# Kernel tuning notes

Measured on AMD Instinct MI355X. Metric: run time of the kernel, lower is better.

The kernel has to match this reference:

```python
import jax, jax.numpy as jnp
import numpy as np
import math

D_MODEL = 2048
N_HEADS = 16
D_K = D_MODEL // N_HEADS


def setup_inputs() -> dict:
    key = jax.random.key(0)
    k0, k1, k2, k3, k4 = jax.random.split(key, 5)
    B, T = 2, 2048
    x = jax.random.normal(k0, (B, T, D_MODEL), dtype=jnp.float32)
    s = 1.0 / math.sqrt(D_MODEL)
    W_qkv = jax.random.normal(k1, (3 * D_MODEL, D_MODEL), dtype=jnp.float32) * s
    b_qkv = jax.random.normal(k2, (3 * D_MODEL,), dtype=jnp.float32) * 0.01
    W_out = jax.random.normal(k3, (D_MODEL, D_MODEL), dtype=jnp.float32) * s
    b_out = jax.random.normal(k4, (D_MODEL,), dtype=jnp.float32) * 0.01
    return {"x": x, "W_qkv": W_qkv, "b_qkv": b_qkv, "W_out": W_out, "b_out": b_out}


def reference(x, W_qkv, b_qkv, W_out, b_out):
    B, T, C = x.shape
    qkv = x @ W_qkv.T + b_qkv                      # [B,T,3C]
    q, k, v = jnp.split(qkv, 3, axis=-1)
    # [B,T,C] -> [B,H,T,Dk]
    def to_heads(t):
        return t.reshape(B, T, N_HEADS, D_K).transpose(0, 2, 1, 3)
    q, k, v = to_heads(q), to_heads(k), to_heads(v)
    scale = 1.0 / math.sqrt(D_K)
    scores = jnp.einsum('bhqd,bhkd->bhqk', q, k) * scale   # [B,H,T,T]
    causal = jnp.tril(jnp.ones((T, T), dtype=bool))
    neg = jnp.finfo(scores.dtype).min
    scores = jnp.where(causal[None, None], scores, neg)
    attn = jax.nn.softmax(scores, axis=-1)
    out = jnp.einsum('bhqk,bhkd->bhqd', attn, v)           # [B,H,T,Dk]
    out = out.transpose(0, 2, 1, 3).reshape(B, T, C)
    return out @ W_out.T + b_out
```

## Files before the change

### kernel.cpp

```cpp
#include <hip/hip_runtime.h>
#include <stdint.h>

typedef short bf16x8 __attribute__((ext_vector_type(8)));
typedef float f32x4 __attribute__((ext_vector_type(4)));
typedef float f32x16 __attribute__((ext_vector_type(16)));
typedef unsigned short u16;
typedef unsigned int u32;

__device__ __forceinline__ u16 f2bf(float f) {
    u32 x = __float_as_uint(f);
    x += 0x7fffu + ((x >> 16) & 1u);
    return (u16)(x >> 16);
}
__device__ __forceinline__ u32 pack_bf2(float a, float b) {
    return (u32)f2bf(a) | ((u32)f2bf(b) << 16);
}
__device__ __forceinline__ float bf2f(u16 v) {
    return __uint_as_float(((u32)v) << 16);
}

union Frag4 { u32 u[4]; bf16x8 v; };

__device__ __forceinline__ void gload16(const u16* g, u16* l) {
    __builtin_amdgcn_global_load_lds(
        (__attribute__((address_space(1))) void*)g,
        (__attribute__((address_space(3))) void*)l,
        16, 0, 0);
}

__global__ void cvt_f32_bf16(const float* __restrict__ in, u16* __restrict__ out, long n8) {
    long stride = (long)gridDim.x * blockDim.x;
    for (long i = (long)blockIdx.x * blockDim.x + threadIdx.x; i < n8; i += stride) {
        const float4* p = (const float4*)(in + i * 8);
        float4 a = p[0], b = p[1];
        uint4 o;
        o.x = pack_bf2(a.x, a.y);
        o.y = pack_bf2(a.z, a.w);
        o.z = pack_bf2(b.x, b.y);
        o.w = pack_bf2(b.z, b.w);
        ((uint4*)out)[i] = o;
    }
}

__global__ __launch_bounds__(512, 2) void gemm128_8w(
    const u16* __restrict__ A, const u16* __restrict__ B,
    const float* __restrict__ bias, u16* __restrict__ out,
    int K, int ldo, int gxsh)
{
    __shared__ __align__(16) u16 lA[2 * 128 * 64];
    __shared__ __align__(16) u16 lB[2 * 128 * 64];
    const int tid  = threadIdx.x;
    const int lane = tid & 63;
    const int w    = tid >> 6;
    const int wm = (w >> 2) * 64;
    const int wn = (w & 3) * 32;

    const int nwg = gridDim.x;
    const int bid = blockIdx.x;
    const int swz = (bid & 7) * (nwg >> 3) + (bid >> 3);
    const int bm = (swz & ((1 << gxsh) - 1)) * 128;
    const int bn = (swz >> gxsh) * 128;

    const int lr = lane >> 3;
    const u32 sb = (u32)((lane & 7) * 16);
    const int NT = K >> 6;

    auto stage = [&](int bb, int k0) {
#pragma unroll
        for (int i = 0; i < 2; ++i) {
            const int c = w * 2 + i;
            const int row = c * 8 + lr;
            const u32 col = (sb ^ ((u32)(row & 7) << 4)) >> 1;
            gload16(A + (size_t)(bm + row) * K + k0 + col, lA + bb * 8192 + c * 512);
            gload16(B + (size_t)(bn + row) * K + k0 + col, lB + bb * 8192 + c * 512);
        }
    };

    f32x4 acc[4][2];
#pragma unroll
    for (int i = 0; i < 4; ++i)
#pragma unroll
        for (int j = 0; j < 2; ++j)
#pragma unroll
            for (int r = 0; r < 4; ++r) acc[i][j][r] = 0.f;

    stage(0, 0);
    stage(1, 64);
    asm volatile("s_waitcnt vmcnt(4)" ::: "memory");
    __builtin_amdgcn_sched_barrier(0);
    __builtin_amdgcn_s_barrier();
    __builtin_amdgcn_sched_barrier(0);

    for (int t = 0; t < NT; ++t) {
        const int cur = t & 1;
        const char* pA = (const char*)(lA + cur * 8192);
        const char* pB = (const char*)(lB + cur * 8192);
#pragma unroll
        for (int kk = 0; kk < 2; ++kk) {
            bf16x8 af[4], bfr[2];
#pragma unroll
            for (int f = 0; f < 4; ++f) {
                const int m = wm + f * 16 + (lane & 15);
                const u32 byt = (u32)(kk * 64 + (lane >> 4) * 16) ^ ((u32)(m & 7) << 4);
                af[f] = *(const bf16x8*)(pA + m * 128 + byt);
            }
#pragma unroll
            for (int j = 0; j < 2; ++j) {
                const int n = wn + j * 16 + (lane & 15);
                const u32 byt = (u32)(kk * 64 + (lane >> 4) * 16) ^ ((u32)(n & 7) << 4);
                bfr[j] = *(const bf16x8*)(pB + n * 128 + byt);
            }
            __builtin_amdgcn_s_setprio(1);
#pragma unroll
            for (int i = 0; i < 4; ++i)
#pragma unroll
                for (int j = 0; j < 2; ++j)
                    acc[i][j] = __builtin_amdgcn_mfma_f32_16x16x32_bf16(af[i], bfr[j], acc[i][j], 0, 0, 0);
            __builtin_amdgcn_s_setprio(0);
        }
        __builtin_amdgcn_sched_barrier(0);
        __builtin_amdgcn_s_barrier();
        __builtin_amdgcn_sched_barrier(0);
        if (t + 2 < NT) {
            stage(cur, (t + 2) * 64);
            asm volatile("s_waitcnt vmcnt(4)" ::: "memory");
        } else {
            asm volatile("s_waitcnt vmcnt(0)" ::: "memory");
        }
        __builtin_amdgcn_sched_barrier(0);
        __builtin_amdgcn_s_barrier();
        __builtin_amdgcn_sched_barrier(0);
    }

#pragma unroll
    for (int i = 0; i < 4; ++i) {
        int m0 = bm + wm + i * 16 + ((lane >> 4) << 2);
#pragma unroll
        for (int j = 0; j < 2; ++j) {
            int n = bn + wn + j * 16 + (lane & 15);
            float bv = bias[n];
#pragma unroll
            for (int r = 0; r < 4; ++r)
                out[(size_t)(m0 + r) * ldo + n] = f2bf(acc[i][j][r] + bv);
        }
    }
}

template<int OBF>
__global__ __launch_bounds__(256, 2) void gemm_nt(
    const u16* __restrict__ A, const u16* __restrict__ B,
    const float* __restrict__ bias, void* __restrict__ out,
    int K, int ldo, int gxsh)
{
    __shared__ __align__(16) u16 lA[2 * 128 * 64];
    __shared__ __align__(16) u16 lB[2 * 128 * 64];
    const int tid  = threadIdx.x;
    const int lane = tid & 63;
    const int w    = tid >> 6;
    const int wm = (w >> 1) * 64, wn = (w & 1) * 64;

    const int nwg = gridDim.x;
    const int bid = blockIdx.x;
    const int swz = (bid & 7) * (nwg >> 3) + (bid >> 3);
    const int bm = (swz & ((1 << gxsh) - 1)) * 128;
    const int bn = (swz >> gxsh) * 128;

    const int lr = lane >> 3;
    const u32 sb = (u32)((lane & 7) * 16);
    const int NT = K >> 6;

    auto stage = [&](int bb, int k0) {
#pragma unroll
        for (int i = 0; i < 4; ++i) {
            const int c = w * 4 + i;
            const int row = c * 8 + lr;
            const u32 col = (sb ^ ((u32)(row & 7) << 4)) >> 1;
            gload16(A + (size_t)(bm + row) * K + k0 + col, lA + bb * 8192 + c * 512);
            gload16(B + (size_t)(bn + row) * K + k0 + col, lB + bb * 8192 + c * 512);
        }
    };

    f32x4 acc[4][4];
#pragma unroll
    for (int i = 0; i < 4; ++i)
#pragma unroll
        for (int j = 0; j < 4; ++j)
#pragma unroll
            for (int r = 0; r < 4; ++r) acc[i][j][r] = 0.f;

    stage(0, 0);
    stage(1, 64);
    asm volatile("s_waitcnt vmcnt(8)" ::: "memory");
    __builtin_amdgcn_sched_barrier(0);
    __builtin_amdgcn_s_barrier();
    __builtin_amdgcn_sched_barrier(0);

    for (int t = 0; t < NT; ++t) {
        const int cur = t & 1;
        const char* pA = (const char*)(lA + cur * 8192);
        const char* pB = (const char*)(lB + cur * 8192);
#pragma unroll
        for (int kk = 0; kk < 2; ++kk) {
            bf16x8 af[4], bfr[4];
#pragma unroll
            for (int f = 0; f < 4; ++f) {
                const int m = wm + f * 16 + (lane & 15);
                const u32 byt = (u32)(kk * 64 + (lane >> 4) * 16) ^ ((u32)(m & 7) << 4);
                af[f]  = *(const bf16x8*)(pA + m * 128 + byt);
                const int n = wn + f * 16 + (lane & 15);
                const u32 bytb = (u32)(kk * 64 + (lane >> 4) * 16) ^ ((u32)(n & 7) << 4);
                bfr[f] = *(const bf16x8*)(pB + n * 128 + bytb);
            }
            __builtin_amdgcn_s_setprio(1);
#pragma unroll
            for (int i = 0; i < 4; ++i)
#pragma unroll
                for (int j = 0; j < 4; ++j)
                    acc[i][j] = __builtin_amdgcn_mfma_f32_16x16x32_bf16(af[i], bfr[j], acc[i][j], 0, 0, 0);
            __builtin_amdgcn_s_setprio(0);
        }
        __builtin_amdgcn_sched_barrier(0);
        __builtin_amdgcn_s_barrier();
        __builtin_amdgcn_sched_barrier(0);
        if (t + 2 < NT) {
            stage(cur, (t + 2) * 64);
            asm volatile("s_waitcnt vmcnt(8)" ::: "memory");
        } else {
            asm volatile("s_waitcnt vmcnt(0)" ::: "memory");
        }
        __builtin_amdgcn_sched_barrier(0);
        __builtin_amdgcn_s_barrier();
        __builtin_amdgcn_sched_barrier(0);
    }

#pragma unroll
    for (int i = 0; i < 4; ++i) {
        int m0 = bm + wm + i * 16 + ((lane >> 4) << 2);
#pragma unroll
        for (int j = 0; j < 4; ++j) {
            int n = bn + wn + j * 16 + (lane & 15);
            float bv = bias[n];
#pragma unroll
            for (int r = 0; r < 4; ++r) {
                float v = acc[i][j][r] + bv;
                if constexpr (OBF != 0)
                    ((u16*)out)[(size_t)(m0 + r) * ldo + n] = f2bf(v);
                else
                    ((float*)out)[(size_t)(m0 + r) * ldo + n] = v;
            }
        }
    }
}

__global__ __launch_bounds__(256) void transpose_v(
    const u16* __restrict__ qkv, u16* __restrict__ vt)
{
    __shared__ u16 lt[64 * 64];
    const int tid = threadIdx.x;
    const int bid = blockIdx.x;
    const int tt    = bid & 31;
    const int dtile = (bid >> 5) & 1;
    const int h     = (bid >> 6) & 15;
    const int b     = bid >> 10;
    const u16* src = qkv + ((size_t)b * 2048 + tt * 64) * 6144 + 4096 + h * 128 + dtile * 64;

    const int r = tid >> 2, ce = (tid & 3) * 16;
    uint4 a0 = *(const uint4*)(src + (size_t)r * 6144 + ce);
    uint4 a1 = *(const uint4*)(src + (size_t)r * 6144 + ce + 8);
    const u32 swz = (u32)((r & 7) << 4);
    *(uint4*)((char*)lt + r * 128 + (((u32)(ce * 2)) ^ swz)) = a0;
    *(uint4*)((char*)lt + r * 128 + (((u32)(ce * 2 + 16)) ^ swz)) = a1;
    __syncthreads();

    const int d = tid >> 2;
    u16* dst = vt + ((size_t)(b * 16 + h) * 128 + dtile * 64 + d) * 2048 + tt * 64;
#pragma unroll
    for (int it = 0; it < 2; ++it) {
        const int t0 = (tid & 3) * 8 + it * 32;
        union { u16 hh[8]; uint4 q4; } u;
#pragma unroll
        for (int uu = 0; uu < 8; ++uu) {
            int trow = t0 + uu;
            u32 byt = (u32)(trow * 128) + (((u32)(d * 2)) ^ ((u32)((trow & 7) << 4)));
            u.hh[uu] = *(const u16*)((const char*)lt + byt);
        }
        *(uint4*)(dst + t0) = u.q4;
    }
}

__constant__ unsigned char QT_TAB[30] = {11,11, 5,15,15,15,10,10,14,14,14, 9, 9, 4,13,13,13,12,12,12, 8, 8, 7, 7, 3, 6, 6, 2, 1, 0};
__constant__ unsigned char TLO_TAB[30]= { 0,24, 0, 0,22,43, 0,22, 0,20,40, 0,20, 0, 0,19,38, 0,18,36, 0,18, 0,16, 0, 0,14, 0, 0, 0};
__constant__ unsigned char THI_TAB[30]= {24,48,24,22,43,64,22,44,20,40,60,20,40,20,19,38,56,18,36,52,18,36,16,32,16,14,28,12, 8, 4};
__constant__ unsigned char SL_TAB[30] = {10,11,255,21,22,23, 8, 9,18,19,20, 6, 7,255,15,16,17,12,13,14, 4, 5, 2, 3,255, 0, 1,255,255,255};

__global__ __launch_bounds__(256) void attn_fwd(
    const u16* __restrict__ qkv, const u16* __restrict__ vt,
    u16* __restrict__ obuf, u16* __restrict__ pout, float* __restrict__ pml)
{
    __shared__ __align__(16) u16 lS[17408];
    const int tid  = threadIdx.x;
    const int lane = tid & 63;
    const int w    = tid >> 6;
    const int g    = lane >> 5;
    const int ql   = lane & 31;

    const int bid  = blockIdx.x;
    const int item = bid >> 5;
    const int bh   = bid & 31;
    const int qt   = QT_TAB[item];
    const int slot = SL_TAB[item];
    const int t_lo = TLO_TAB[item];
    const int t_hi = THI_TAB[item];
    const int b = bh >> 4, h = bh & 15;
    const size_t rowbase = (size_t)b * 2048;
    const int qb = qt * 128;
    const int qw = qb + w * 32;
    const int q  = qw + ql;

    const u16* Khead = qkv + rowbase * 6144 + 2048 + h * 128;
    const u16* Vth   = vt + (size_t)bh * 128 * 2048;

    bf16x8 qf[8];
    {
        const u16* qrow = qkv + (rowbase + q) * 6144 + h * 128;
#pragma unroll
        for (int ch = 0; ch < 8; ++ch)
            qf[ch] = *(const bf16x8*)(qrow + ch * 16 + g * 8);
    }

    f32x16 acc[4];
#pragma unroll
    for (int dt = 0; dt < 4; ++dt)
#pragma unroll
        for (int r = 0; r < 16; ++r) acc[dt][r] = 0.f;

    float m_run = -1e30f, l_run = 0.f;
    const float C2 = 0.08838834764831845f * 1.44269504088896341f;

    auto stage = [&](int bb, int t) {
        const int kb = t * 32;
#pragma unroll
        for (int i = 0; i < 2; ++i) {
            const int c = w * 2 + i;
            const int kr = c * 4 + (lane >> 4);
            const u32 kcol = (((u32)((lane & 15) * 16)) ^ ((u32)(kr & 7) << 4)) >> 1;
            gload16(Khead + (size_t)(kb + kr) * 6144 + kcol,
                    lS + bb * 4096 + c * 512);
            const int vr = c * 16 + (lane >> 2);
            const u32 vcol = (((u32)((lane & 3) * 16)) ^ ((u32)(vr & 3) << 4)) >> 1;
            gload16(Vth + (size_t)vr * 2048 + kb + vcol,
                    lS + 8192 + bb * 4096 + c * 512);
        }
    };

    stage(0, t_lo);
    __syncthreads();
    int buf = 0;

    for (int t = t_lo; t < t_hi; ++t) {
        const int kb = t * 32;
        if (t + 1 < t_hi) stage(buf ^ 1, t + 1);

        if (kb <= qw + 31) {
            const char* lKb = (const char*)(lS + buf * 4096);
            const char* lVb = (const char*)(lS + 8192 + buf * 4096);
            const bool diag = (kb == qw);

            bf16x8 kf[8];
            const u32 ksw = ((u32)ql & 7) << 4;
#pragma unroll
            for (int ch = 0; ch < 8; ++ch)
                kf[ch] = *(const bf16x8*)(lKb + ql * 256 + (((u32)(ch * 32 + g * 16)) ^ ksw));

            f32x16 s_;
#pragma unroll
            for (int r = 0; r < 16; ++r) s_[r] = 0.f;
            __builtin_amdgcn_s_setprio(1);
#pragma unroll
            for (int ch = 0; ch < 8; ++ch)
                s_ = __builtin_amdgcn_mfma_f32_32x32x16_bf16(kf[ch], qf[ch], s_, 0, 0, 0);
            __builtin_amdgcn_s_setprio(0);

            float p[16];
            float tmax = -1e30f;
#pragma unroll
            for (int r = 0; r < 16; ++r) {
                int crow = (r & 3) + 8 * (r >> 2) + 4 * g;
                float v = s_[r];
                if (diag && (crow > ql)) v = -1e30f;
                p[r] = v;
                tmax = fmaxf(tmax, v);
            }
            tmax = fmaxf(tmax, __shfl_xor(tmax, 32));
            if (!__all(tmax <= m_run + 8.0f)) {
                float mnew  = fmaxf(m_run, tmax);
                float alpha = exp2f((m_run - mnew) * C2);
#pragma unroll
                for (int dt = 0; dt < 4; ++dt) acc[dt] = acc[dt] * alpha;
                l_run *= alpha;
                m_run = mnew;
            }
            float ssum = 0.f;
#pragma unroll
            for (int r = 0; r < 16; ++r) {
                float e = exp2f((p[r] - m_run) * C2);
                p[r] = e;
                ssum += e;
            }
            ssum += __shfl_xor(ssum, 32);
            l_run += ssum;

            u32 wb[8], sw[8];
#pragma unroll
            for (int j = 0; j < 8; ++j) wb[j] = pack_bf2(p[2 * j], p[2 * j + 1]);
#pragma unroll
            for (int j = 0; j < 8; ++j) sw[j] = __shfl_xor(wb[j], 32);
            Frag4 pf0, pf1;
#pragma unroll
            for (int u = 0; u < 4; ++u) {
                const bool own = (g == (u >> 1));
                pf0.u[u] = own ? wb[2 * g + (u & 1)]     : sw[2 * g + (u & 1)];
                pf1.u[u] = own ? wb[4 + 2 * g + (u & 1)] : sw[4 + 2 * g + (u & 1)];
            }

            __builtin_amdgcn_s_setprio(1);
#pragma unroll
            for (int dt = 0; dt < 4; ++dt) {
                const u32 vrow = (u32)(dt * 32 + ql);
                const u32 vsw = (vrow & 3) << 4;
                bf16x8 v0 = *(const bf16x8*)(lVb + vrow * 64 + (((u32)(g * 16)) ^ vsw));
                bf16x8 v1 = *(const bf16x8*)(lVb + vrow * 64 + (((u32)(32 + g * 16)) ^ vsw));
                acc[dt] = __builtin_amdgcn_mfma_f32_32x32x16_bf16(v0, pf0.v, acc[dt], 0, 0, 0);
                acc[dt] = __builtin_amdgcn_mfma_f32_32x32x16_bf16(v1, pf1.v, acc[dt], 0, 0, 0);
            }
            __builtin_amdgcn_s_setprio(0);
        }
        __syncthreads();
        buf ^= 1;
    }

    const float scale = (slot == 255) ? (1.0f / l_run) : 1.0f;
    u16* lO = lS + w * 4352;
#pragma unroll
    for (int dt = 0; dt < 4; ++dt) {
#pragma unroll
        for (int rr = 0; rr < 4; ++rr) {
            int d0 = dt * 32 + rr * 8 + g * 4;
            int r0 = rr * 4;
            u32* dst = (u32*)(lO + ql * 136 + d0);
            dst[0] = pack_bf2(acc[dt][r0] * scale,     acc[dt][r0 + 1] * scale);
            dst[1] = pack_bf2(acc[dt][r0 + 2] * scale, acc[dt][r0 + 3] * scale);
        }
    }
    if (slot != 255 && g == 0) {
        const int sg = bh * 24 + slot;
        float2* pm = (float2*)pml + sg * 128 + (w * 32 + ql);
        *pm = make_float2(m_run, l_run);
    }
    __syncthreads();

    u16* gbase;
    size_t rstride;
    if (slot == 255) {
        gbase = obuf + (rowbase + qw) * 2048 + h * 128;
        rstride = 2048;
    } else {
        const int sg = bh * 24 + slot;
        gbase = pout + (size_t)sg * 16384 + (size_t)(w * 32) * 128;
        rstride = 128;
    }
    const int eo = (lane & 15) * 8;
#pragma unroll
    for (int pass = 0; pass < 8; ++pass) {
        const int row = pass * 4 + (lane >> 4);
        bf16x8 v = *(const bf16x8*)(lO + row * 136 + eo);
        *(bf16x8*)(gbase + (size_t)row * rstride + eo) = v;
    }
}

__global__ __launch_bounds__(256) void attn_merge(
    const u16* __restrict__ pout, const float* __restrict__ pml,
    u16* __restrict__ obuf)
{
    const int bid = blockIdx.x;
    const int bh = bid & 31, j = bid >> 5;
    const int qt = 6 + j;
    const int b = bh >> 4, h = bh & 15;
    const int tid = threadIdx.x;
    const int f  = (qt < 12) ? 2 : 3;
    const int sb = (qt < 12) ? (qt - 6) * 2 : 12 + (qt - 12) * 3;
    const int base = bh * 24 + sb;
    const float C2 = 0.08838834764831845f * 1.44269504088896341f;
    const int eo = (tid & 15) * 8;

#pragma unroll
    for (int pass = 0; pass < 8; ++pass) {
        const int row = pass * 16 + (tid >> 4);
        float mv[3], lv[3], wv[3];
        float ms = -1e30f;
#pragma unroll
        for (int i = 0; i < 3; ++i) {
            if (i < f) {
                float2 ml = ((const float2*)pml)[(base + i) * 128 + row];
                mv[i] = ml.x; lv[i] = ml.y;
                ms = fmaxf(ms, ml.x);
            }
        }
        float L = 0.f;
#pragma unroll
        for (int i = 0; i < 3; ++i) {
            if (i < f) {
                wv[i] = exp2f((mv[i] - ms) * C2);
                L += lv[i] * wv[i];
            }
        }
        const float inv = 1.0f / L;

        float o[8];
#pragma unroll
        for (int e = 0; e < 8; ++e) o[e] = 0.f;
#pragma unroll
        for (int i = 0; i < 3; ++i) {
            if (i < f) {
                bf16x8 v = *(const bf16x8*)(pout + (size_t)(base + i) * 16384
                                            + (size_t)row * 128 + eo);
#pragma unroll
                for (int e = 0; e < 8; ++e) o[e] += wv[i] * bf2f((u16)v[e]);
            }
        }
        u16* orow = obuf + ((size_t)b * 2048 + qt * 128 + row) * 2048 + h * 128 + eo;
#pragma unroll
        for (int e = 0; e < 8; e += 2)
            *(u32*)(orow + e) = pack_bf2(o[e] * inv, o[e + 1] * inv);
    }
}

extern "C" void kernel_launch(void* const* d_in, const int* in_sizes, int n_in,
                              void* d_out, int out_size, void* d_ws, size_t ws_size,
                              hipStream_t stream) {
    (void)in_sizes; (void)n_in; (void)out_size; (void)ws_size;
    const float* x    = (const float*)d_in[0];
    const float* Wqkv = (const float*)d_in[1];
    const float* bqkv = (const float*)d_in[2];
    const float* Wout = (const float*)d_in[3];
    const float* bout = (const float*)d_in[4];

    char* ws = (char*)d_ws;
    u16* xb  = (u16*)ws;
    u16* wqb = (u16*)(ws + (size_t)16777216);
    u16* qkv = (u16*)(ws + (size_t)41943040);
    u16* ob  = xb;
    u16* vtb = wqb;
    u16* wob = wqb;
    float* pml = (float*)(ws + (size_t)33554432);
    u16* pO  = (u16*)d_out;

    cvt_f32_bf16<<<2048, 256, 0, stream>>>(x, xb, 8388608L / 8);
    cvt_f32_bf16<<<2048, 256, 0, stream>>>(Wqkv, wqb, 12582912L / 8);
    gemm128_8w<<<1536, 512, 0, stream>>>(xb, wqb, bqkv, qkv, 2048, 6144, 5);
    transpose_v<<<2048, 256, 0, stream>>>(qkv, vtb);
    attn_fwd<<<960, 256, 0, stream>>>(qkv, vtb, ob, pO, pml);
    attn_merge<<<320, 256, 0, stream>>>(pO, pml, ob);
    cvt_f32_bf16<<<2048, 256, 0, stream>>>(Wout, wob, 4194304L / 8);
    gemm_nt<0><<<512, 256, 0, stream>>>(ob, wob, bout, d_out, 2048, 2048, 5);
}
```

Baseline: 300.0 us.

## Fuse input conversions, restructure QKV GEMM pipeline, use 8-wave out-projection

```diff
diff --git a/kernel.cpp b/kernel.cpp
--- a/kernel.cpp
+++ b/kernel.cpp
@@ -42,9 +42,30 @@
     }
 }
 
-__global__ __launch_bounds__(512, 2) void gemm128_8w(
+__global__ void cvt2_f32_bf16(const float* __restrict__ inA, u16* __restrict__ outA, long n8A,
+                              const float* __restrict__ inB, u16* __restrict__ outB, long n8B) {
+    long stride = (long)gridDim.x * blockDim.x;
+    const long tot = n8A + n8B;
+    for (long i = (long)blockIdx.x * blockDim.x + threadIdx.x; i < tot; i += stride) {
+        const float4* p;
+        uint4* q;
+        if (i < n8A) { p = (const float4*)(inA + i * 8);        q = (uint4*)outA + i; }
+        else         { long j = i - n8A;
+                       p = (const float4*)(inB + j * 8);        q = (uint4*)outB + j; }
+        float4 a = p[0], b = p[1];
+        uint4 o;
+        o.x = pack_bf2(a.x, a.y);
+        o.y = pack_bf2(a.z, a.w);
+        o.z = pack_bf2(b.x, b.y);
+        o.w = pack_bf2(b.z, b.w);
+        *q = o;
+    }
+}
+
+template<int OBF>
+__global__ __launch_bounds__(512, 2) void gemm128_1b(
     const u16* __restrict__ A, const u16* __restrict__ B,
-    const float* __restrict__ bias, u16* __restrict__ out,
+    const float* __restrict__ bias, void* __restrict__ out,
     int K, int ldo, int gxsh)
 {
     __shared__ __align__(16) u16 lA[2 * 128 * 64];
@@ -85,14 +106,16 @@
             for (int r = 0; r < 4; ++r) acc[i][j][r] = 0.f;
 
     stage(0, 0);
-    stage(1, 64);
-    asm volatile("s_waitcnt vmcnt(4)" ::: "memory");
+    asm volatile("s_waitcnt vmcnt(0)" ::: "memory");
     __builtin_amdgcn_sched_barrier(0);
     __builtin_amdgcn_s_barrier();
     __builtin_amdgcn_sched_barrier(0);
 
+    int cur = 0;
     for (int t = 0; t < NT; ++t) {
-        const int cur = t & 1;
+        if (t + 1 < NT) stage(cur ^ 1, (t + 1) * 64);
+        __builtin_amdgcn_sched_barrier(0);
+
         const char* pA = (const char*)(lA + cur * 8192);
         const char* pB = (const char*)(lB + cur * 8192);
 #pragma unroll
@@ -118,18 +141,11 @@
                     acc[i][j] = __builtin_amdgcn_mfma_f32_16x16x32_bf16(af[i], bfr[j], acc[i][j], 0, 0, 0);
             __builtin_amdgcn_s_setprio(0);
         }
+        asm volatile("s_waitcnt vmcnt(0)" ::: "memory");
         __builtin_amdgcn_sched_barrier(0);
         __builtin_amdgcn_s_barrier();
         __builtin_amdgcn_sched_barrier(0);
-        if (t + 2 < NT) {
-            stage(cur, (t + 2) * 64);
-            asm volatile("s_waitcnt vmcnt(4)" ::: "memory");
-        } else {
-            asm volatile("s_waitcnt vmcnt(0)" ::: "memory");
-        }
-        __builtin_amdgcn_sched_barrier(0);
-        __builtin_amdgcn_s_barrier();
-        __builtin_amdgcn_sched_barrier(0);
+        cur ^= 1;
     }
 
 #pragma unroll
@@ -140,14 +156,19 @@
             int n = bn + wn + j * 16 + (lane & 15);
             float bv = bias[n];
 #pragma unroll
-            for (int r = 0; r < 4; ++r)
-                out[(size_t)(m0 + r) * ldo + n] = f2bf(acc[i][j][r] + bv);
+            for (int r = 0; r < 4; ++r) {
+                float v = acc[i][j][r] + bv;
+                if constexpr (OBF != 0)
+                    ((u16*)out)[(size_t)(m0 + r) * ldo + n] = f2bf(v);
+                else
+                    ((float*)out)[(size_t)(m0 + r) * ldo + n] = v;
+            }
         }
     }
 }
 
 template<int OBF>
-__global__ __launch_bounds__(256, 2) void gemm_nt(
+__global__ __launch_bounds__(512, 2) void gemm128_8w(
     const u16* __restrict__ A, const u16* __restrict__ B,
     const float* __restrict__ bias, void* __restrict__ out,
     int K, int ldo, int gxsh)
@@ -157,7 +178,8 @@
     const int tid  = threadIdx.x;
     const int lane = tid & 63;
     const int w    = tid >> 6;
-    const int wm = (w >> 1) * 64, wn = (w & 1) * 64;
+    const int wm = (w >> 2) * 64;
+    const int wn = (w & 3) * 32;
 
     const int nwg = gridDim.x;
     const int bid = blockIdx.x;
@@ -171,8 +193,8 @@
 
     auto stage = [&](int bb, int k0) {
 #pragma unroll
-        for (int i = 0; i < 4; ++i) {
-            const int c = w * 4 + i;
+        for (int i = 0; i < 2; ++i) {
+            const int c = w * 2 + i;
             const int row = c * 8 + lr;
             const u32 col = (sb ^ ((u32)(row & 7) << 4)) >> 1;
             gload16(A + (size_t)(bm + row) * K + k0 + col, lA + bb * 8192 + c * 512);
@@ -180,17 +202,17 @@
         }
     };
 
-    f32x4 acc[4][4];
+    f32x4 acc[4][2];
 #pragma unroll
     for (int i = 0; i < 4; ++i)
 #pragma unroll
-        for (int j = 0; j < 4; ++j)
+        for (int j = 0; j < 2; ++j)
 #pragma unroll
             for (int r = 0; r < 4; ++r) acc[i][j][r] = 0.f;
 
     stage(0, 0);
     stage(1, 64);
-    asm volatile("s_waitcnt vmcnt(8)" ::: "memory");
+    asm volatile("s_waitcnt vmcnt(4)" ::: "memory");
     __builtin_amdgcn_sched_barrier(0);
     __builtin_amdgcn_s_barrier();
     __builtin_amdgcn_sched_barrier(0);
@@ -201,21 +223,24 @@
         const char* pB = (const char*)(lB + cur * 8192);
 #pragma unroll
         for (int kk = 0; kk < 2; ++kk) {
-            bf16x8 af[4], bfr[4];
+            bf16x8 af[4], bfr[2];
 #pragma unroll
             for (int f = 0; f < 4; ++f) {
                 const int m = wm + f * 16 + (lane & 15);
                 const u32 byt = (u32)(kk * 64 + (lane >> 4) * 16) ^ ((u32)(m & 7) << 4);
-                af[f]  = *(const bf16x8*)(pA + m * 128 + byt);
-                const int n = wn + f * 16 + (lane & 15);
-                const u32 bytb = (u32)(kk * 64 + (lane >> 4) * 16) ^ ((u32)(n & 7) << 4);
-                bfr[f] = *(const bf16x8*)(pB + n * 128 + bytb);
+                af[f] = *(const bf16x8*)(pA + m * 128 + byt);
+            }
+#pragma unroll
+            for (int j = 0; j < 2; ++j) {
+                const int n = wn + j * 16 + (lane & 15);
+                const u32 byt = (u32)(kk * 64 + (lane >> 4) * 16) ^ ((u32)(n & 7) << 4);
+                bfr[j] = *(const bf16x8*)(pB + n * 128 + byt);
             }
             __builtin_amdgcn_s_setprio(1);
 #pragma unroll
             for (int i = 0; i < 4; ++i)
 #pragma unroll
-                for (int j = 0; j < 4; ++j)
+                for (int j = 0; j < 2; ++j)
                     acc[i][j] = __builtin_amdgcn_mfma_f32_16x16x32_bf16(af[i], bfr[j], acc[i][j], 0, 0, 0);
             __builtin_amdgcn_s_setprio(0);
         }
@@ -224,7 +249,7 @@
         __builtin_amdgcn_sched_barrier(0);
         if (t + 2 < NT) {
             stage(cur, (t + 2) * 64);
-            asm volatile("s_waitcnt vmcnt(8)" ::: "memory");
+            asm volatile("s_waitcnt vmcnt(4)" ::: "memory");
         } else {
             asm volatile("s_waitcnt vmcnt(0)" ::: "memory");
         }
@@ -237,7 +262,7 @@
     for (int i = 0; i < 4; ++i) {
         int m0 = bm + wm + i * 16 + ((lane >> 4) << 2);
 #pragma unroll
-        for (int j = 0; j < 4; ++j) {
+        for (int j = 0; j < 2; ++j) {
             int n = bn + wn + j * 16 + (lane & 15);
             float bv = bias[n];
 #pragma unroll
@@ -555,12 +580,12 @@
     float* pml = (float*)(ws + (size_t)33554432);
     u16* pO  = (u16*)d_out;
 
-    cvt_f32_bf16<<<2048, 256, 0, stream>>>(x, xb, 8388608L / 8);
-    cvt_f32_bf16<<<2048, 256, 0, stream>>>(Wqkv, wqb, 12582912L / 8);
-    gemm128_8w<<<1536, 512, 0, stream>>>(xb, wqb, bqkv, qkv, 2048, 6144, 5);
+    cvt2_f32_bf16<<<2048, 256, 0, stream>>>(x, xb, 8388608L / 8,
+                                            Wqkv, wqb, 12582912L / 8);
+    gemm128_1b<1><<<1536, 512, 0, stream>>>(xb, wqb, bqkv, qkv, 2048, 6144, 5);
     transpose_v<<<2048, 256, 0, stream>>>(qkv, vtb);
     attn_fwd<<<960, 256, 0, stream>>>(qkv, vtb, ob, pO, pml);
     attn_merge<<<320, 256, 0, stream>>>(pO, pml, ob);
     cvt_f32_bf16<<<2048, 256, 0, stream>>>(Wout, wob, 4194304L / 8);
-    gemm_nt<0><<<512, 256, 0, stream>>>(ob, wob, bout, d_out, 2048, 2048, 5);
-}
+    gemm128_8w<0><<<512, 512, 0, stream>>>(ob, wob, bout, d_out, 2048, 2048, 5);
+}
```

Result: no change. 297.5 us (-0.8%).
